# Optimization experiments

Measured on AMD Instinct MI355X. Metric: run time of the kernel, lower is better.

Reference implementation:

```python
import jax, jax.numpy as jnp
import numpy as np


def conv2d(x, w, pad, groups=1):
    # x: [B,Cin,H,W], w: [Cout,Cin/groups,K,K]
    return jax.lax.conv_general_dilated(
        x, w, (1, 1), [(pad, pad), (pad, pad)],
        dimension_numbers=('NCHW', 'OIHW', 'NCHW'),
        feature_group_count=groups)


def setup_inputs() -> dict:
    key = jax.random.key(0)
    ks = jax.random.split(key, 24)
    B, C, H, W = 16, 512, 32, 128          # batch, encoder_dim, feature map
    Da, Ds, De, Dm = 512, 256, 256, 1024   # att_dim, state_dim, embed_dim, mem_dim
    V, Dmerge = 1000, 512
    K, P = 11, 5
    Din = De + C + Dm                       # GRU input dim = 1792
    s = 0.02
    rn = lambda k, shp, sc=1.0: jax.random.normal(k, shp, jnp.float32) * sc
    return {
        'encode': rn(ks[0], (B, C, H, W)),
        'encode_pro': rn(ks[1], (B, Da, H, W)),
        'encode_mask': jnp.ones((B, 1, H, W), jnp.float32),
        'state': rn(ks[2], (B, Ds)),
        'pre_weight': jax.random.uniform(ks[3], (B, 1, H, W), jnp.float32),
        'cum_weight': jax.random.uniform(ks[4], (B, 1, H, W), jnp.float32),
        'context': rn(ks[5], (B, C)),
        'cond_mem': rn(ks[6], (B, Dm)),
        'cond_weight': jax.random.uniform(ks[7], (B, 2, H, W), jnp.float32),
        'label_id': jax.random.randint(ks[8], (B,), 0, V),
        # ImageAttention params (all bias-free per source)
        'w_wt': rn(ks[9], (Da, 1, K, K), s),
        'w_cwt': rn(ks[10], (Da, 1, K, K), s),
        'w_condwt': rn(ks[11], (2 * Da, 1, K, K), s),   # groups=2
        'w_energy': rn(ks[12], (Da,), s),               # 1x1 conv -> vector
        'w_state': rn(ks[13], (Da, Ds), s),
        'w_ctx': rn(ks[14], (Da, C), s),
        'w_cond': rn(ks[15], (Da, Dm), s),
        # GRU params
        'w_i2s': rn(ks[16], (Ds, Din), s), 'b_i2s': jnp.zeros((Ds,), jnp.float32),
        'w_i2g': rn(ks[17], (2 * Ds, Din), s), 'b_i2g': jnp.zeros((2 * Ds,), jnp.float32),
        'w_s2g': rn(ks[18], (2 * Ds, Ds), s),
        'w_h2h': rn(ks[19], (Ds, Ds), s),
        # Readout params
        'embed_table': rn(ks[20], (V, De), s),
        'w_l1': rn(ks[21], (Dmerge, De + Ds + C), s), 'b_l1': jnp.zeros((Dmerge,), jnp.float32),
        'w_l2': rn(ks[22], (V, Dmerge), s), 'b_l2': jnp.zeros((V,), jnp.float32),
    }


def reference(encode, encode_pro, encode_mask, state, pre_weight, cum_weight,
              context, cond_mem, cond_weight, label_id, w_wt, w_cwt, w_condwt,
              w_energy, w_state, w_ctx, w_cond, w_i2s, b_i2s, w_i2g, b_i2g,
              w_s2g, w_h2h, embed_table, w_l1, b_l1, w_l2, b_l2):
    P = (w_wt.shape[-1] - 1) // 2
    Da = w_energy.shape[0]
    B, C, H, W = encode.shape
    # --- ImageAttention ---
    t_pre = conv2d(pre_weight, w_wt, P)           # [B,Da,H,W]
    t_cum = conv2d(cum_weight, w_cwt, P)          # [B,Da,H,W]
    t_cw = conv2d(cond_weight, w_condwt, P, groups=2)
    t_cw = t_cw.reshape(B, 2, Da, H, W).sum(1)    # [B,Da,H,W]
    st = state @ w_state.T + context @ w_ctx.T + cond_mem @ w_cond.T  # [B,Da]
    concat_info = jnp.tanh(st[:, :, None, None] + t_pre + t_cum + t_cw + encode_pro)
    energies = jnp.einsum('bchw,c->bhw', concat_info, w_energy)
    energies = energies + (encode_mask[:, 0] - 1.0) * 1e8
    att = jax.nn.softmax(energies.reshape(B, H * W), axis=1)
    new_weight = att.reshape(B, 1, H, W)
    new_cum_weight = cum_weight + new_weight
    ctx = jnp.einsum('bchw,bhw->bc', encode, new_weight[:, 0])  # [B,C]
    # --- GRU transition (data = [embed, ctx, cond_mem]) ---
    embed = embed_table[label_id]
    data = jnp.concatenate([embed, ctx, cond_mem], axis=1)
    gate = data @ w_i2g.T + b_i2g + state @ w_s2g.T
    Ds = state.shape[1]
    update_g = jax.nn.sigmoid(gate[:, :Ds])
    reset_g = jax.nn.sigmoid(gate[:, Ds:])
    state_hat = jnp.tanh(data @ w_i2s.T + b_i2s + (state * reset_g) @ w_h2h.T)
    new_state = update_g * state_hat + (1.0 - update_g) * state
    # --- Readout.step ---
    merged = jnp.concatenate([embed, new_state, ctx], axis=1)
    hid = jax.nn.relu(merged @ w_l1.T + b_l1)
    readout = hid @ w_l2.T + b_l2                  # [B,V]
    return readout
```

## Files before the change

kernel.cpp:

```cpp
#include <hip/hip_runtime.h>
#include <math.h>

typedef unsigned short u16;
typedef __bf16 bf16x8 __attribute__((ext_vector_type(8)));
typedef float f32x4 __attribute__((ext_vector_type(4)));

__device__ u16   g_A_pack[16 * 512 * 32];
__device__ float g_st[16 * 512];
__device__ float g_eraw[16 * 4096];
__device__ float g_energ[16 * 4096];
__device__ float g_data[16 * 1792];
__device__ float g_merged[16 * 1024];
__device__ float g_update[16 * 256];
__device__ float g_reset[16 * 256];
__device__ float g_i2s[16 * 256];
__device__ float g_hid[16 * 512];

__device__ __forceinline__ u16 f2bf(float f) {
    unsigned u = __float_as_uint(f);
    u = (u + 0x7FFFu + ((u >> 16) & 1u)) >> 16;
    return (u16)u;
}
__device__ __forceinline__ float fast_tanh(float x) {
    return 1.0f - 2.0f / (__expf(2.0f * x) + 1.0f);
}
__device__ __forceinline__ float sigmoidf_(float x) {
    return 1.0f / (1.0f + __expf(-x));
}

__global__ void k_prep(const float* __restrict__ w_wt, const float* __restrict__ w_cwt,
                       const float* __restrict__ w_condwt) {
    int idx = blockIdx.x * blockDim.x + threadIdx.x;
    if (idx >= 512 * 512) return;
    int d = idx >> 9, k = idx & 511;
    float f = 0.f;
    if (k < 484) {
        int c = k / 121, rem = k % 121;
        if (c == 0)      f = w_wt[d * 121 + rem];
        else if (c == 1) f = w_cwt[d * 121 + rem];
        else if (c == 2) f = w_condwt[d * 121 + rem];
        else             f = w_condwt[(512 + d) * 121 + rem];
    }
    int ks = k >> 5, kl = k & 31;
    g_A_pack[(ks * 512 + d) * 32 + kl] = f2bf(f);
}

__global__ void k_st(const float* __restrict__ state, const float* __restrict__ context,
                     const float* __restrict__ cond_mem, const float* __restrict__ w_state,
                     const float* __restrict__ w_ctx, const float* __restrict__ w_cond) {
    int wid = (blockIdx.x * blockDim.x + threadIdx.x) >> 6;
    int lane = threadIdx.x & 63;
    if (wid >= 16 * 512) return;
    int b = wid >> 9, d = wid & 511;
    float acc = 0.f;
    for (int k = lane; k < 256; k += 64)  acc += state[b * 256 + k]    * w_state[d * 256 + k];
    for (int k = lane; k < 512; k += 64)  acc += context[b * 512 + k]  * w_ctx[d * 512 + k];
    for (int k = lane; k < 1024; k += 64) acc += cond_mem[b * 1024 + k] * w_cond[d * 1024 + k];
    for (int off = 32; off; off >>= 1) acc += __shfl_down(acc, off, 64);
    if (lane == 0) g_st[b * 512 + d] = acc;
}

__global__ void k_e0(const int* __restrict__ label, const float* __restrict__ embed_table,
                     const float* __restrict__ cond_mem) {
    int b = blockIdx.x, tid = threadIdx.x;
    int lbl = label[b];
    if (tid < 256) {
        float ev = embed_table[lbl * 256 + tid];
        g_data[b * 1792 + tid] = ev;
        g_merged[b * 1024 + tid] = ev;
    }
    for (int k = tid; k < 1024; k += 256)
        g_data[b * 1792 + 768 + k] = cond_mem[b * 1024 + k];
}

__global__ __launch_bounds__(512, 2) void k_conv_energy(
    const float* __restrict__ pre_w, const float* __restrict__ cum_w, const float* __restrict__ cond_w,
    const float* __restrict__ encode_pro, const float* __restrict__ w_energy)
{
    __shared__ __align__(16) u16 src[4][11][80];
    __shared__ __align__(16) u16 bchunk[64][520];
    __shared__ float ered[8][64];

    const int blk = blockIdx.x;
    const int pxh = blk & 1;
    const int h = (blk >> 1) & 31;
    const int b = blk >> 6;
    const int px0 = pxh * 64;

    const int tid = threadIdx.x;
    const int lane = tid & 63, wv = tid >> 6;
    const int lr = lane & 15, lg = lane >> 4;

    for (int t = tid; t < 4 * 11 * 80; t += 512) {
        int c = t / (11 * 80);
        int rem = t % (11 * 80);
        int i = rem / 80, x = rem % 80;
        int row = h + i - 5, w = px0 - 5 + x;
        u16 v = 0;
        if (x < 74 && row >= 0 && row < 32 && w >= 0 && w < 128) {
            const float* img = (c == 0) ? pre_w + b * 4096
                             : (c == 1) ? cum_w + b * 4096
                             : (c == 2) ? cond_w + b * 8192
                                        : cond_w + b * 8192 + 4096;
            v = f2bf(img[row * 128 + w]);
        }
        src[c][i][x] = v;
    }
    __syncthreads();

    {
        const int k = tid;
        if (k < 484) {
            int c = k / 121, rem = k % 121;
            int i = rem / 11, jj = rem % 11;
            const u16* s = &src[c][i][jj];
#pragma unroll 8
            for (int n = 0; n < 64; ++n) bchunk[n][k] = s[n];
        } else {
#pragma unroll 8
            for (int n = 0; n < 64; ++n) bchunk[n][k] = 0;
        }
    }
    __syncthreads();

    f32x4 acc[4][4];
#pragma unroll
    for (int mt = 0; mt < 4; ++mt)
#pragma unroll
        for (int nt = 0; nt < 4; ++nt) {
            f32x4 z = {0.f, 0.f, 0.f, 0.f};
            acc[mt][nt] = z;
        }

#pragma unroll 2
    for (int ks = 0; ks < 16; ++ks) {
        bf16x8 afr[4];
#pragma unroll
        for (int mt = 0; mt < 4; ++mt) {
            int d = wv * 64 + mt * 16 + lr;
            afr[mt] = *reinterpret_cast<const bf16x8*>(&g_A_pack[(ks * 512 + d) * 32 + lg * 8]);
        }
        bf16x8 bfr[4];
#pragma unroll
        for (int nt = 0; nt < 4; ++nt)
            bfr[nt] = *reinterpret_cast<const bf16x8*>(&bchunk[nt * 16 + lr][ks * 32 + lg * 8]);

#pragma unroll
        for (int mt = 0; mt < 4; ++mt)
#pragma unroll
            for (int nt = 0; nt < 4; ++nt)
                acc[mt][nt] = __builtin_amdgcn_mfma_f32_16x16x32_bf16(afr[mt], bfr[nt], acc[mt][nt], 0, 0, 0);
    }

    float e[4] = {0.f, 0.f, 0.f, 0.f};
#pragma unroll
    for (int mt = 0; mt < 4; ++mt) {
#pragma unroll
        for (int r = 0; r < 4; ++r) {
            int d = wv * 64 + mt * 16 + lg * 4 + r;
            float stv = g_st[b * 512 + d];
            float wev = w_energy[d];
            const float* ep_row = encode_pro + ((size_t)(b * 512 + d) * 32 + h) * 128 + px0;
#pragma unroll
            for (int nt = 0; nt < 4; ++nt) {
                float val = stv + acc[mt][nt][r] + ep_row[nt * 16 + lr];
                e[nt] += wev * fast_tanh(val);
            }
        }
    }
#pragma unroll
    for (int nt = 0; nt < 4; ++nt) {
        float v = e[nt];
        v += __shfl_xor(v, 16, 64);
        v += __shfl_xor(v, 32, 64);
        if (lane < 16) ered[wv][nt * 16 + lane] = v;
    }
    __syncthreads();
    if (tid < 64) {
        float v = 0.f;
#pragma unroll
        for (int w = 0; w < 8; ++w) v += ered[w][tid];
        g_eraw[b * 4096 + h * 128 + px0 + tid] = v;
    }
}

__global__ void k_softmax(const float* __restrict__ encode_mask) {
    __shared__ float red[256];
    int b = blockIdx.x, tid = threadIdx.x;
    float v[16];
    float mx = -1e30f;
#pragma unroll
    for (int i = 0; i < 16; ++i) {
        int idx = b * 4096 + tid + i * 256;
        float ev = g_eraw[idx] + (encode_mask[idx] - 1.0f) * 1e8f;
        v[i] = ev; mx = fmaxf(mx, ev);
    }
    red[tid] = mx; __syncthreads();
    for (int s = 128; s; s >>= 1) { if (tid < s) red[tid] = fmaxf(red[tid], red[tid + s]); __syncthreads(); }
    mx = red[0]; __syncthreads();
    float sum = 0.f;
#pragma unroll
    for (int i = 0; i < 16; ++i) { v[i] = __expf(v[i] - mx); sum += v[i]; }
    red[tid] = sum; __syncthreads();
    for (int s = 128; s; s >>= 1) { if (tid < s) red[tid] += red[tid + s]; __syncthreads(); }
    float inv = 1.0f / red[0];
#pragma unroll
    for (int i = 0; i < 16; ++i) g_energ[b * 4096 + tid + i * 256] = v[i] * inv;
}

__global__ void k_ctx(const float* __restrict__ encode) {
    int wid = (blockIdx.x * blockDim.x + threadIdx.x) >> 6;
    int lane = threadIdx.x & 63;
    if (wid >= 16 * 512) return;
    int b = wid >> 9, c = wid & 511;
    const float* e = encode + (size_t)wid * 4096;
    const float* a = g_energ + b * 4096;
    float acc = 0.f;
#pragma unroll
    for (int it = 0; it < 16; ++it) {
        int base = it * 256 + lane * 4;
        float4 ev = *reinterpret_cast<const float4*>(&e[base]);
        float4 av = *reinterpret_cast<const float4*>(&a[base]);
        acc += ev.x * av.x + ev.y * av.y + ev.z * av.z + ev.w * av.w;
    }
    for (int off = 32; off; off >>= 1) acc += __shfl_down(acc, off, 64);
    if (lane == 0) { g_data[b * 1792 + 256 + c] = acc; g_merged[b * 1024 + 512 + c] = acc; }
}

__global__ void k_e1(const float* __restrict__ state,
                     const float* __restrict__ w_i2g, const float* __restrict__ b_i2g,
                     const float* __restrict__ w_s2g, const float* __restrict__ w_i2s,
                     const float* __restrict__ b_i2s) {
    int wid = (blockIdx.x * blockDim.x + threadIdx.x) >> 6;
    int lane = threadIdx.x & 63;
    if (wid >= 16 * 768) return;
    int b = wid / 768, o = wid % 768;
    const float* dt = g_data + b * 1792;
    float acc = 0.f;
    if (o < 512) {
        const float* wr = w_i2g + o * 1792;
        for (int k = lane; k < 1792; k += 64) acc += dt[k] * wr[k];
        const float* wsg = w_s2g + o * 256;
        for (int k = lane; k < 256; k += 64) acc += state[b * 256 + k] * wsg[k];
    } else {
        const float* wr = w_i2s + (o - 512) * 1792;
        for (int k = lane; k < 1792; k += 64) acc += dt[k] * wr[k];
    }
    for (int off = 32; off; off >>= 1) acc += __shfl_down(acc, off, 64);
    if (lane == 0) {
        if (o < 256)       g_update[b * 256 + o]        = sigmoidf_(acc + b_i2g[o]);
        else if (o < 512)  g_reset[b * 256 + (o - 256)] = sigmoidf_(acc + b_i2g[o]);
        else               g_i2s[b * 256 + (o - 512)]   = acc + b_i2s[o - 512];
    }
}

__global__ void k_e2(const float* __restrict__ state, const float* __restrict__ w_h2h) {
    int wid = (blockIdx.x * blockDim.x + threadIdx.x) >> 6;
    int lane = threadIdx.x & 63;
    if (wid >= 16 * 256) return;
    int b = wid >> 8, d = wid & 255;
    const float* wr = w_h2h + d * 256;
    float acc = 0.f;
    for (int k = lane; k < 256; k += 64)
        acc += state[b * 256 + k] * g_reset[b * 256 + k] * wr[k];
    for (int off = 32; off; off >>= 1) acc += __shfl_down(acc, off, 64);
    if (lane == 0) {
        float sh = fast_tanh(g_i2s[b * 256 + d] + acc);
        float u = g_update[b * 256 + d];
        g_merged[b * 1024 + 256 + d] = u * sh + (1.f - u) * state[b * 256 + d];
    }
}

__global__ void k_e3(const float* __restrict__ w_l1, const float* __restrict__ b_l1) {
    int wid = (blockIdx.x * blockDim.x + threadIdx.x) >> 6;
    int lane = threadIdx.x & 63;
    if (wid >= 16 * 512) return;
    int b = wid >> 9, m = wid & 511;
    const float* mg = g_merged + b * 1024;
    const float* wr = w_l1 + m * 1024;
    float acc = 0.f;
    for (int k = lane; k < 1024; k += 64) acc += mg[k] * wr[k];
    for (int off = 32; off; off >>= 1) acc += __shfl_down(acc, off, 64);
    if (lane == 0) g_hid[b * 512 + m] = fmaxf(acc + b_l1[m], 0.f);
}

__global__ void k_e4(const float* __restrict__ w_l2, const float* __restrict__ b_l2,
                     float* __restrict__ out) {
    int wid = (blockIdx.x * blockDim.x + threadIdx.x) >> 6;
    int lane = threadIdx.x & 63;
    if (wid >= 16 * 1000) return;
    int b = wid / 1000, v = wid % 1000;
    const float* hd = g_hid + b * 512;
    const float* wr = w_l2 + v * 512;
    float acc = 0.f;
    for (int k = lane; k < 512; k += 64) acc += hd[k] * wr[k];
    for (int off = 32; off; off >>= 1) acc += __shfl_down(acc, off, 64);
    if (lane == 0) out[b * 1000 + v] = acc + b_l2[v];
}

extern "C" void kernel_launch(void* const* d_in, const int* in_sizes, int n_in,
                              void* d_out, int out_size, void* d_ws, size_t ws_size,
                              hipStream_t stream) {
    static const int EXP[28] = {
        33554432, 33554432, 65536, 4096, 65536, 65536, 8192, 16384, 131072, 16,
        61952, 61952, 123904, 512, 131072, 262144, 524288, 458752, 256, 917504,
        512, 131072, 65536, 256000, 524288, 512, 512000, 1000};
    if (n_in != 28) return;
    for (int i = 0; i < 28; ++i)
        if (in_sizes[i] != EXP[i]) return;

    const float* encode      = (const float*)d_in[0];
    const float* encode_pro  = (const float*)d_in[1];
    const float* encode_mask = (const float*)d_in[2];
    const float* state       = (const float*)d_in[3];
    const float* pre_weight  = (const float*)d_in[4];
    const float* cum_weight  = (const float*)d_in[5];
    const float* context     = (const float*)d_in[6];
    const float* cond_mem    = (const float*)d_in[7];
    const float* cond_weight = (const float*)d_in[8];
    const int*   label_id    = (const int*)d_in[9];
    const float* w_wt     = (const float*)d_in[10];
    const float* w_cwt    = (const float*)d_in[11];
    const float* w_condwt = (const float*)d_in[12];
    const float* w_energy = (const float*)d_in[13];
    const float* w_state  = (const float*)d_in[14];
    const float* w_ctx    = (const float*)d_in[15];
    const float* w_cond   = (const float*)d_in[16];
    const float* w_i2s    = (const float*)d_in[17];
    const float* b_i2s    = (const float*)d_in[18];
    const float* w_i2g    = (const float*)d_in[19];
    const float* b_i2g    = (const float*)d_in[20];
    const float* w_s2g    = (const float*)d_in[21];
    const float* w_h2h    = (const float*)d_in[22];
    const float* embed_t  = (const float*)d_in[23];
    const float* w_l1     = (const float*)d_in[24];
    const float* b_l1     = (const float*)d_in[25];
    const float* w_l2     = (const float*)d_in[26];
    const float* b_l2     = (const float*)d_in[27];
    float* out = (float*)d_out;
    (void)d_ws; (void)ws_size;

    k_prep<<<1024, 256, 0, stream>>>(w_wt, w_cwt, w_condwt);
    k_st<<<2048, 256, 0, stream>>>(state, context, cond_mem, w_state, w_ctx, w_cond);
    k_e0<<<16, 256, 0, stream>>>(label_id, embed_t, cond_mem);
    k_conv_energy<<<1024, 512, 0, stream>>>(pre_weight, cum_weight, cond_weight,
                                            encode_pro, w_energy);
    k_softmax<<<16, 256, 0, stream>>>(encode_mask);
    k_ctx<<<2048, 256, 0, stream>>>(encode);
    k_e1<<<3072, 256, 0, stream>>>(state, w_i2g, b_i2g, w_s2g, w_i2s, b_i2s);
    k_e2<<<1024, 256, 0, stream>>>(state, w_h2h);
    k_e3<<<2048, 256, 0, stream>>>(w_l1, b_l1);
    k_e4<<<4000, 256, 0, stream>>>(w_l2, b_l2, out);
}
```

Baseline: 194.5 us.

## Prefetch encode_pro tile into LDS and double-buffer im2col B-chunks

```diff
diff --git a/kernel.cpp b/kernel.cpp
--- a/kernel.cpp
+++ b/kernel.cpp
@@ -73,12 +73,13 @@
         g_data[b * 1792 + 768 + k] = cond_mem[b * 1024 + k];
 }
 
-__global__ __launch_bounds__(512, 2) void k_conv_energy(
+__global__ __launch_bounds__(512, 1) void k_conv_energy(
     const float* __restrict__ pre_w, const float* __restrict__ cum_w, const float* __restrict__ cond_w,
     const float* __restrict__ encode_pro, const float* __restrict__ w_energy)
 {
     __shared__ __align__(16) u16 src[4][11][80];
-    __shared__ __align__(16) u16 bchunk[64][520];
+    __shared__ __align__(16) u16 bchunk[2][64][40];
+    __shared__ __align__(16) float epro_lds[512 * 64];
     __shared__ float ered[8][64];
 
     const int blk = blockIdx.x;
@@ -91,37 +92,52 @@
     const int lane = tid & 63, wv = tid >> 6;
     const int lr = lane & 15, lg = lane >> 4;
 
-    for (int t = tid; t < 4 * 11 * 80; t += 512) {
-        int c = t / (11 * 80);
-        int rem = t % (11 * 80);
-        int i = rem / 80, x = rem % 80;
-        int row = h + i - 5, w = px0 - 5 + x;
-        u16 v = 0;
-        if (x < 74 && row >= 0 && row < 32 && w >= 0 && w < 128) {
-            const float* img = (c == 0) ? pre_w + b * 4096
-                             : (c == 1) ? cum_w + b * 4096
-                             : (c == 2) ? cond_w + b * 8192
-                                        : cond_w + b * 8192 + 4096;
-            v = f2bf(img[row * 128 + w]);
-        }
-        src[c][i][x] = v;
+    {
+        const float* epbase = encode_pro + (size_t)b * 512 * 4096 + h * 128 + px0;
+#pragma unroll
+        for (int i = 0; i < 16; ++i) {
+            int o = i * 2048 + tid * 4;
+            int r = o >> 6, c = o & 63;
+            float4 v = *reinterpret_cast<const float4*>(&epbase[(size_t)r * 4096 + c]);
+            *reinterpret_cast<float4*>(&epro_lds[o]) = v;
+        }
+    }
+
+#pragma unroll
+    for (int it = 0; it < 7; ++it) {
+        int t = tid + it * 512;
+        if (t < 4 * 11 * 80) {
+            int c = t / (11 * 80);
+            int rem = t % (11 * 80);
+            int i = rem / 80, x = rem % 80;
+            int row = h + i - 5, w = px0 - 5 + x;
+            u16 v = 0;
+            if (x < 74 && row >= 0 && row < 32 && w >= 0 && w < 128) {
+                const float* img = (c == 0) ? pre_w + b * 4096
+                                 : (c == 1) ? cum_w + b * 4096
+                                 : (c == 2) ? cond_w + b * 8192
+                                            : cond_w + b * 8192 + 4096;
+                v = f2bf(img[row * 128 + w]);
+            }
+            src[c][i][x] = v;
+        }
     }
     __syncthreads();
 
-    {
-        const int k = tid;
-        if (k < 484) {
-            int c = k / 121, rem = k % 121;
-            int i = rem / 11, jj = rem % 11;
-            const u16* s = &src[c][i][jj];
-#pragma unroll 8
-            for (int n = 0; n < 64; ++n) bchunk[n][k] = s[n];
-        } else {
-#pragma unroll 8
-            for (int n = 0; n < 64; ++n) bchunk[n][k] = 0;
-        }
-    }
-    __syncthreads();
+    const int kl = tid & 31;
+    const int n0 = tid >> 5;
+#define BUILD(KS, BUF)                                                          \
+    {                                                                           \
+        int kg = (KS) * 32 + kl;                                                \
+        int c = 0, i = 0, jj = 0;                                               \
+        bool ok = (kg < 484);                                                   \
+        if (ok) { c = kg / 121; int r2 = kg % 121; i = r2 / 11; jj = r2 % 11; } \
+        _Pragma("unroll")                                                       \
+        for (int rep = 0; rep < 4; ++rep) {                                     \
+            int n = n0 + rep * 16;                                              \
+            bchunk[BUF][n][kl] = ok ? src[c][i][n + jj] : (u16)0;               \
+        }                                                                       \
+    }
 
     f32x4 acc[4][4];
 #pragma unroll
@@ -132,8 +148,11 @@
             acc[mt][nt] = z;
         }
 
-#pragma unroll 2
+    BUILD(0, 0);
+    __syncthreads();
+
     for (int ks = 0; ks < 16; ++ks) {
+        const int cur = ks & 1;
         bf16x8 afr[4];
 #pragma unroll
         for (int mt = 0; mt < 4; ++mt) {
@@ -143,14 +162,18 @@
         bf16x8 bfr[4];
 #pragma unroll
         for (int nt = 0; nt < 4; ++nt)
-            bfr[nt] = *reinterpret_cast<const bf16x8*>(&bchunk[nt * 16 + lr][ks * 32 + lg * 8]);
+            bfr[nt] = *reinterpret_cast<const bf16x8*>(&bchunk[cur][nt * 16 + lr][lg * 8]);
+
+        if (ks < 15) BUILD(ks + 1, cur ^ 1);
 
 #pragma unroll
         for (int mt = 0; mt < 4; ++mt)
 #pragma unroll
             for (int nt = 0; nt < 4; ++nt)
                 acc[mt][nt] = __builtin_amdgcn_mfma_f32_16x16x32_bf16(afr[mt], bfr[nt], acc[mt][nt], 0, 0, 0);
-    }
+        __syncthreads();
+    }
+#undef BUILD
 
     float e[4] = {0.f, 0.f, 0.f, 0.f};
 #pragma unroll
@@ -160,10 +183,10 @@
             int d = wv * 64 + mt * 16 + lg * 4 + r;
             float stv = g_st[b * 512 + d];
             float wev = w_energy[d];
-            const float* ep_row = encode_pro + ((size_t)(b * 512 + d) * 32 + h) * 128 + px0;
 #pragma unroll
             for (int nt = 0; nt < 4; ++nt) {
-                float val = stv + acc[mt][nt][r] + ep_row[nt * 16 + lr];
+                int px = nt * 16 + lr;
+                float val = stv + acc[mt][nt][r] + epro_lds[d * 64 + px];
                 e[nt] += wev * fast_tanh(val);
             }
         }
```

After: 194.3 us. Within noise of the previous version (-0.1%).
